# Kernel tuning notes

Hardware: AMD Instinct MI355X
Metric: run time of the kernel (lower is better)

## Reference

```python
import jax, jax.numpy as jnp
import numpy as np

N_FFT = 1024
N_STAGES = 4
BATCH = 16384


def _mod_seq(order):
    mset = [0]
    for o in range(order):
        step = 2 ** o
        mset = [v for x in mset for v in (x, x + step)]
    return mset


def _partial_bit_reversal(N, order):
    m = np.zeros((N, N), dtype=np.float32)
    base = 2 ** order
    k = 0
    for p in _mod_seq(order):
        for j in range(N // base):
            m[j * base + p, k] = 1.0
            k += 1
    return m


def setup_inputs() -> dict:
    key = jax.random.key(0)
    x = jax.random.normal(key, (BATCH, N_FFT), dtype=jnp.float32)
    n_sub = N_FFT // 2 ** N_STAGES  # 64: dense sub-DFT size
    dft = np.fft.fft(np.eye(n_sub))
    inp = {
        "x": x,
        "perm": jnp.asarray(_partial_bit_reversal(N_FFT, N_STAGES)),
        "fft_real": jnp.asarray(dft.real, dtype=jnp.float32),
        "fft_imag": jnp.asarray(dft.imag, dtype=jnp.float32),
    }
    stage = N_FFT // 2 ** (N_STAGES - 1)  # 128, doubles each stage
    for s in range(N_STAGES):
        w = np.exp(-2j * np.pi / stage) ** np.arange(stage // 2)
        inp[f"tw_real_{s}"] = jnp.asarray(w.real, dtype=jnp.float32)
        inp[f"tw_imag_{s}"] = jnp.asarray(w.imag, dtype=jnp.float32)
        stage *= 2
    return inp


def _fft_forward(x, perm, fft_real, fft_imag, tws):
    # bit-reversal permutation (matmul against 0/1 matrix, as in the original)
    y = x @ perm
    n_chunks = 2 ** N_STAGES
    # stack chunks: (n_chunks, B, n_sub)
    c = jnp.stack(jnp.split(y, n_chunks, axis=-1), axis=0)
    ev, od = c[0::2], c[1::2]  # (m, B, s) each, m = n_chunks // 2
    # dense sub-DFTs (x @ M.T)
    ev_r = jnp.einsum('mbs,ts->mbt', ev, fft_real)
    ev_i = jnp.einsum('mbs,ts->mbt', ev, fft_imag)
    od_r = jnp.einsum('mbs,ts->mbt', od, fft_real)
    od_i = jnp.einsum('mbs,ts->mbt', od, fft_imag)
    # butterfly twiddle stages; m halves and s doubles each stage
    for tr, ti in tws:
        todd_r = tr * od_r - ti * od_i
        todd_i = tr * od_i + ti * od_r
        real = jnp.concatenate([ev_r + todd_r, ev_r - todd_r], axis=-1)
        imag = jnp.concatenate([ev_i + todd_i, ev_i - todd_i], axis=-1)
        ev_r, od_r = real[0::2], real[1::2]
        ev_i, od_i = imag[0::2], imag[1::2]
    return ev_r[0], ev_i[0]


def reference(x, perm, fft_real, fft_imag,
              tw_real_0, tw_imag_0, tw_real_1, tw_imag_1,
              tw_real_2, tw_imag_2, tw_real_3, tw_imag_3):
    tws = [(tw_real_0, tw_imag_0), (tw_real_1, tw_imag_1),
           (tw_real_2, tw_imag_2), (tw_real_3, tw_imag_3)]
    return _fft_forward(x, perm, fft_real, fft_imag, tws)
```

## Files before the change

### kernel.cpp

```cpp
#include <hip/hip_runtime.h>


#define N_FFT 1024
#define BATCH 16384
#define TPB   256

__device__ __forceinline__ int pad16(int a) { return a + (a >> 4); }

__device__ __forceinline__ float2 cmul(float2 a, float2 b) {
    return make_float2(a.x * b.x - a.y * b.y, a.x * b.y + a.y * b.x);
}

template<int M, int STEP>
__device__ __forceinline__ void stage_mid(const float2* __restrict__ src,
                                          float2* __restrict__ dst,
                                          const float2* __restrict__ tw,
                                          int tid)
{
    const int j = tid / M;
    const int k = tid % M;
    float2 a = src[pad16(tid)];
    float2 b = src[pad16(tid + 256)];
    float2 c = src[pad16(tid + 512)];
    float2 d = src[pad16(tid + 768)];
    float2 t0 = make_float2(a.x + c.x, a.y + c.y);
    float2 t1 = make_float2(a.x - c.x, a.y - c.y);
    float2 t2 = make_float2(b.x + d.x, b.y + d.y);
    float2 t3 = make_float2(b.y - d.y, d.x - b.x);
    float2 y0 = make_float2(t0.x + t2.x, t0.y + t2.y);
    float2 u1 = make_float2(t1.x + t3.x, t1.y + t3.y);
    float2 u2 = make_float2(t0.x - t2.x, t0.y - t2.y);
    float2 u3 = make_float2(t1.x - t3.x, t1.y - t3.y);
    float2 w1 = tw[STEP * j];
    float2 w2 = tw[2 * STEP * j];
    float2 w3 = tw[3 * STEP * j];
    const int base = 4 * M * j + k;
    dst[pad16(base)]         = y0;
    dst[pad16(base + M)]     = cmul(u1, w1);
    dst[pad16(base + 2 * M)] = cmul(u2, w2);
    dst[pad16(base + 3 * M)] = cmul(u3, w3);
}

__global__ __launch_bounds__(TPB) void fft1024_kernel(
    const float* __restrict__ x,
    const float* __restrict__ twr,
    const float* __restrict__ twi,
    float* __restrict__ outr,
    float* __restrict__ outi)
{
    __shared__ float2 bufA[1088];
    __shared__ float2 bufB[1088];
    __shared__ float2 tw[1024];

    const int tid = threadIdx.x;
    const long long row = blockIdx.x;

    for (int i = tid; i < 512; i += TPB) {
        float r = twr[i], im = twi[i];
        tw[i]       = make_float2(r, im);
        tw[i + 512] = make_float2(-r, -im);
    }
    __syncthreads();

    const float* __restrict__ xr = x + row * N_FFT;

    {
        float a = xr[tid];
        float b = xr[tid + 256];
        float c = xr[tid + 512];
        float d = xr[tid + 768];
        float t0 = a + c, t1 = a - c;
        float t2 = b + d, t3 = d - b;
        float2 w1 = tw[tid];
        float2 w2 = tw[2 * tid];
        float2 w3 = tw[3 * tid];
        const int base = 4 * tid;
        bufA[pad16(base)]     = make_float2(t0 + t2, 0.0f);
        bufA[pad16(base + 1)] = make_float2(t1 * w1.x - t3 * w1.y,
                                            t1 * w1.y + t3 * w1.x);
        bufA[pad16(base + 2)] = make_float2((t0 - t2) * w2.x,
                                            (t0 - t2) * w2.y);
        bufA[pad16(base + 3)] = make_float2(t1 * w3.x + t3 * w3.y,
                                            t1 * w3.y - t3 * w3.x);
    }
    __syncthreads();

    stage_mid<4, 4>(bufA, bufB, tw, tid);
    __syncthreads();
    stage_mid<16, 16>(bufB, bufA, tw, tid);
    __syncthreads();
    stage_mid<64, 64>(bufA, bufB, tw, tid);
    __syncthreads();

    {
        float2 a = bufB[pad16(tid)];
        float2 b = bufB[pad16(tid + 256)];
        float2 c = bufB[pad16(tid + 512)];
        float2 d = bufB[pad16(tid + 768)];
        float2 t0 = make_float2(a.x + c.x, a.y + c.y);
        float2 t1 = make_float2(a.x - c.x, a.y - c.y);
        float2 t2 = make_float2(b.x + d.x, b.y + d.y);
        float2 t3 = make_float2(b.y - d.y, d.x - b.x);
        float* __restrict__ orow = outr + row * N_FFT;
        float* __restrict__ irow = outi + row * N_FFT;
        orow[tid]       = t0.x + t2.x;  irow[tid]       = t0.y + t2.y;
        orow[tid + 256] = t1.x + t3.x;  irow[tid + 256] = t1.y + t3.y;
        orow[tid + 512] = t0.x - t2.x;  irow[tid + 512] = t0.y - t2.y;
        orow[tid + 768] = t1.x - t3.x;  irow[tid + 768] = t1.y - t3.y;
    }
}

extern "C" void kernel_launch(void* const* d_in, const int* in_sizes, int n_in,
                              void* d_out, int out_size, void* d_ws, size_t ws_size,
                              hipStream_t stream) {
    const float* x   = (const float*)d_in[0];
    const float* twr = (const float*)d_in[10];
    const float* twi = (const float*)d_in[11];
    float* outr = (float*)d_out;
    float* outi = outr + (size_t)BATCH * N_FFT;
    fft1024_kernel<<<BATCH, TPB, 0, stream>>>(x, twr, twi, outr, outi);
}
```

Baseline: 207.8 us.

## Pack two real rows into one complex FFT and split spectra after

Each block now treats two real input rows as the real and imaginary parts of one complex signal. It runs a single complex 1024-point FFT and separates the two spectra using conjugate symmetry. This halves the number of blocks and the per-row FFT arithmetic and twiddle-table setup. In exchange it adds a full fifth radix-4 stage through shared memory plus one more barrier, and the first stage now does complex work. The final loads read mirrored indices, which may cause LDS bank conflicts.

```diff
diff --git a/kernel.cpp b/kernel.cpp
--- a/kernel.cpp
+++ b/kernel.cpp
@@ -12,17 +12,13 @@
 }
 
 template<int M, int STEP>
-__device__ __forceinline__ void stage_mid(const float2* __restrict__ src,
-                                          float2* __restrict__ dst,
-                                          const float2* __restrict__ tw,
-                                          int tid)
+__device__ __forceinline__ void butterfly_store(float2 a, float2 b, float2 c, float2 d,
+                                                float2* __restrict__ dst,
+                                                const float2* __restrict__ tw,
+                                                int tid)
 {
     const int j = tid / M;
     const int k = tid % M;
-    float2 a = src[pad16(tid)];
-    float2 b = src[pad16(tid + 256)];
-    float2 c = src[pad16(tid + 512)];
-    float2 d = src[pad16(tid + 768)];
     float2 t0 = make_float2(a.x + c.x, a.y + c.y);
     float2 t1 = make_float2(a.x - c.x, a.y - c.y);
     float2 t2 = make_float2(b.x + d.x, b.y + d.y);
@@ -41,6 +37,19 @@
     dst[pad16(base + 3 * M)] = cmul(u3, w3);
 }
 
+template<int M, int STEP>
+__device__ __forceinline__ void stage_mid(const float2* __restrict__ src,
+                                          float2* __restrict__ dst,
+                                          const float2* __restrict__ tw,
+                                          int tid)
+{
+    float2 a = src[pad16(tid)];
+    float2 b = src[pad16(tid + 256)];
+    float2 c = src[pad16(tid + 512)];
+    float2 d = src[pad16(tid + 768)];
+    butterfly_store<M, STEP>(a, b, c, d, dst, tw, tid);
+}
+
 __global__ __launch_bounds__(TPB) void fft1024_kernel(
     const float* __restrict__ x,
     const float* __restrict__ twr,
@@ -53,35 +62,24 @@
     __shared__ float2 tw[1024];
 
     const int tid = threadIdx.x;
-    const long long row = blockIdx.x;
+    const long long r0 = 2LL * blockIdx.x;
 
     for (int i = tid; i < 512; i += TPB) {
-        float r = twr[i], im = twi[i];
-        tw[i]       = make_float2(r, im);
-        tw[i + 512] = make_float2(-r, -im);
+        float re = twr[i], im = twi[i];
+        tw[i]       = make_float2(re, im);
+        tw[i + 512] = make_float2(-re, -im);
     }
     __syncthreads();
 
-    const float* __restrict__ xr = x + row * N_FFT;
+    const float* __restrict__ x0 = x + r0 * N_FFT;
+    const float* __restrict__ x1 = x0 + N_FFT;
 
     {
-        float a = xr[tid];
-        float b = xr[tid + 256];
-        float c = xr[tid + 512];
-        float d = xr[tid + 768];
-        float t0 = a + c, t1 = a - c;
-        float t2 = b + d, t3 = d - b;
-        float2 w1 = tw[tid];
-        float2 w2 = tw[2 * tid];
-        float2 w3 = tw[3 * tid];
-        const int base = 4 * tid;
-        bufA[pad16(base)]     = make_float2(t0 + t2, 0.0f);
-        bufA[pad16(base + 1)] = make_float2(t1 * w1.x - t3 * w1.y,
-                                            t1 * w1.y + t3 * w1.x);
-        bufA[pad16(base + 2)] = make_float2((t0 - t2) * w2.x,
-                                            (t0 - t2) * w2.y);
-        bufA[pad16(base + 3)] = make_float2(t1 * w3.x + t3 * w3.y,
-                                            t1 * w3.y - t3 * w3.x);
+        float2 a = make_float2(x0[tid],       x1[tid]);
+        float2 b = make_float2(x0[tid + 256], x1[tid + 256]);
+        float2 c = make_float2(x0[tid + 512], x1[tid + 512]);
+        float2 d = make_float2(x0[tid + 768], x1[tid + 768]);
+        butterfly_store<1, 1>(a, b, c, d, bufA, tw, tid);
     }
     __syncthreads();
 
@@ -91,22 +89,23 @@
     __syncthreads();
     stage_mid<64, 64>(bufA, bufB, tw, tid);
     __syncthreads();
+    stage_mid<256, 0>(bufB, bufA, tw, tid);
+    __syncthreads();
 
-    {
-        float2 a = bufB[pad16(tid)];
-        float2 b = bufB[pad16(tid + 256)];
-        float2 c = bufB[pad16(tid + 512)];
-        float2 d = bufB[pad16(tid + 768)];
-        float2 t0 = make_float2(a.x + c.x, a.y + c.y);
-        float2 t1 = make_float2(a.x - c.x, a.y - c.y);
-        float2 t2 = make_float2(b.x + d.x, b.y + d.y);
-        float2 t3 = make_float2(b.y - d.y, d.x - b.x);
-        float* __restrict__ orow = outr + row * N_FFT;
-        float* __restrict__ irow = outi + row * N_FFT;
-        orow[tid]       = t0.x + t2.x;  irow[tid]       = t0.y + t2.y;
-        orow[tid + 256] = t1.x + t3.x;  irow[tid + 256] = t1.y + t3.y;
-        orow[tid + 512] = t0.x - t2.x;  irow[tid + 512] = t0.y - t2.y;
-        orow[tid + 768] = t1.x - t3.x;  irow[tid + 768] = t1.y - t3.y;
+    float* __restrict__ or0 = outr + r0 * N_FFT;
+    float* __restrict__ oi0 = outi + r0 * N_FFT;
+    float* __restrict__ or1 = or0 + N_FFT;
+    float* __restrict__ oi1 = oi0 + N_FFT;
+    #pragma unroll
+    for (int q = 0; q < 4; ++q) {
+        const int k  = tid + q * 256;
+        const int nk = (N_FFT - k) & (N_FFT - 1);
+        float2 zk = bufA[pad16(k)];
+        float2 zn = bufA[pad16(nk)];
+        or0[k] = 0.5f * (zk.x + zn.x);
+        oi0[k] = 0.5f * (zk.y - zn.y);
+        or1[k] = 0.5f * (zk.y + zn.y);
+        oi1[k] = 0.5f * (zn.x - zk.x);
     }
 }
 
@@ -118,5 +117,5 @@
     const float* twi = (const float*)d_in[11];
     float* outr = (float*)d_out;
     float* outi = outr + (size_t)BATCH * N_FFT;
-    fft1024_kernel<<<BATCH, TPB, 0, stream>>>(x, twr, twi, outr, outi);
+    fft1024_kernel<<<BATCH / 2, TPB, 0, stream>>>(x, twr, twi, outr, outi);
 }
```

Measured after the change: 206.1 us. Within noise of the previous version (-0.8%).
